# Kernel optimization log

Hardware: AMD Instinct MI355X
Metric: run time of the kernel (lower is better)

Reference implementation:

```python
import jax, jax.numpy as jnp
import numpy as np

N = 10000
F_IN = 512
HID = 256
C = 16
N_POST_ITER = 4


def setup_inputs() -> dict:
    key = jax.random.key(0)
    ks = jax.random.split(key, 10)
    raw_adj = jax.random.uniform(ks[0], (N, N), dtype=jnp.float32) * 0.01
    A = jax.random.uniform(ks[1], (N, N), dtype=jnp.float32)
    normed_adj = A / jnp.sum(A, axis=1, keepdims=True)  # row-sum-one normalized
    features = jax.random.normal(ks[2], (N, F_IN), dtype=jnp.float32)
    labels = jax.random.randint(ks[3], (N,), 0, C)
    y_onehot = jax.nn.one_hot(labels, C, dtype=jnp.float32)
    train_mask = jax.random.randint(ks[4], (N,), 0, 2).astype(jnp.bool_)
    # GCN belief estimator params (glorot-ish scaling)
    W1 = jax.random.normal(ks[5], (F_IN, HID), dtype=jnp.float32) / np.sqrt(F_IN)
    b1 = jnp.zeros((HID,), dtype=jnp.float32)
    W2 = jax.random.normal(ks[6], (HID, C), dtype=jnp.float32) / np.sqrt(HID)
    b2 = jnp.zeros((C,), dtype=jnp.float32)
    # class-compatibility matrix H (initialized, zero-centered as in init_H)
    H = jax.random.normal(ks[7], (C, C), dtype=jnp.float32) * 0.1
    return {"raw_adj": raw_adj, "normed_adj": normed_adj, "features": features,
            "y_onehot": y_onehot, "train_mask": train_mask,
            "W1": W1, "b1": b1, "W2": W2, "b2": b2, "H": H}


def reference(raw_adj, normed_adj, features, y_onehot, train_mask, W1, b1, W2, b2, H):
    num_class = y_onehot.shape[1]
    # 2-layer GCN belief estimator: adj @ (x @ W) + b
    h = jax.nn.relu(normed_adj @ (features @ W1) + b1)          # [N, HID]
    logits = normed_adj @ (h @ W2) + b2                          # [N, C]
    # post_process: iterative compatibility-guided belief propagation
    prior_belief = jax.nn.softmax(logits, axis=1)
    E_hat = prior_belief - 1.0 / num_class
    B_hat = E_hat
    for _ in range(N_POST_ITER):
        B_hat = E_hat + raw_adj @ (B_hat @ H)
    post_belief = B_hat + 1.0 / num_class
    return post_belief
```

## Files before the change

### kernel.cpp

```cpp
#include <hip/hip_runtime.h>

#define NN 10000
#define KP 10048
static constexpr float INV_C = 1.0f / 16.0f;

typedef __attribute__((ext_vector_type(8))) short bf16x8;
typedef __attribute__((ext_vector_type(4))) float f32x4;
typedef unsigned short u16;
typedef unsigned int u32;

__device__ __forceinline__ u16 f2b(float f) {
    union { float f; u32 u; } v; v.f = f;
    u32 r = v.u + 0x7FFFu + ((v.u >> 16) & 1u);
    return (u16)(r >> 16);
}
__device__ __forceinline__ float b2f(u16 b) {
    union { u32 u; float f; } v; v.u = ((u32)b) << 16;
    return v.f;
}

#define AS1(p) ((__attribute__((address_space(1))) void*)(p))
#define AS3(p) ((__attribute__((address_space(3))) void*)(p))

__global__ __launch_bounds__(256)
void cvt_pad(const float* __restrict__ src, u16* __restrict__ dst)
{
    int c8 = blockIdx.x * 256 + threadIdx.x;
    if (c8 >= KP / 8) return;
    int row = blockIdx.y;
    bf16x8 o;
    if (c8 < NN / 8) {
        const float4* s4 = (const float4*)(src + (size_t)row * NN + c8 * 8);
        float4 a = s4[0], b = s4[1];
        o[0]=f2b(a.x); o[1]=f2b(a.y); o[2]=f2b(a.z); o[3]=f2b(a.w);
        o[4]=f2b(b.x); o[5]=f2b(b.y); o[6]=f2b(b.z); o[7]=f2b(b.w);
    } else {
        o = bf16x8{0,0,0,0,0,0,0,0};
    }
    *(bf16x8*)(dst + (size_t)row * KP + c8 * 8) = o;
}

__global__ __launch_bounds__(256)
void cvt_feat(const float* __restrict__ src, u16* __restrict__ dst)
{
    int c = blockIdx.x * 256 + threadIdx.x;
    size_t base = (size_t)c * 8;
    const float4* s4 = (const float4*)(src + base);
    float4 a = s4[0], b = s4[1];
    bf16x8 o;
    o[0]=f2b(a.x); o[1]=f2b(a.y); o[2]=f2b(a.z); o[3]=f2b(a.w);
    o[4]=f2b(b.x); o[5]=f2b(b.y); o[6]=f2b(b.z); o[7]=f2b(b.w);
    *(bf16x8*)(dst + base) = o;
}

__global__ __launch_bounds__(256)
void w12t(const float* __restrict__ W1, const float* __restrict__ W2,
          float* __restrict__ W1T, u16* __restrict__ W2T)
{
    int bid = blockIdx.x, t = threadIdx.x;
    if (bid < 512) {
        int idx = bid * 256 + t;
        int n = idx >> 9, k = idx & 511;
        W1T[idx] = W1[(size_t)k * 256 + n];
    } else {
        int idx = (bid - 512) * 256 + t;
        if (idx < 4096) {
            int n_ = idx >> 8, k_ = idx & 255;
            W2T[idx] = f2b(W2[(size_t)k_ * 16 + n_]);
        }
    }
}

template<int BIAS, int RELU>
__global__ __launch_bounds__(256)
void gemm_a32_bt16(const float* __restrict__ A, int lda, int M, int Ka,
                   const u16* __restrict__ BT, int ldb, int N, int npad,
                   const float* __restrict__ bias,
                   u16* __restrict__ C, int ldc, int K)
{
    __shared__ u16 Asm[64 * 64];
    __shared__ u16 Bsm[256 * 64];
    const int t = threadIdx.x;
    const int lane = t & 63;
    const int w = t >> 6;
    const int row0 = blockIdx.x * 64;
    const int n0 = blockIdx.y * 256;

    const f32x4 fz = {0.f, 0.f, 0.f, 0.f};
    f32x4 acc[4][4];
#pragma unroll
    for (int i = 0; i < 4; ++i)
#pragma unroll
        for (int j = 0; j < 4; ++j) acc[i][j] = fz;

    const int ar = t >> 2, akq = t & 3;
    int agr = row0 + ar; if (agr > M - 1) agr = M - 1;
    const float* asrc = A + (size_t)agr * lda + akq * 16;
    const int aslot0 = (akq * 2) ^ (ar & 7);
    const int aslot1 = (akq * 2 + 1) ^ (ar & 7);

    const int l8 = lane >> 3, sl = lane & 7;

    for (int k0 = 0; k0 < K; k0 += 64) {
#pragma unroll
        for (int i = 0; i < 8; ++i) {
            int lr = i * 32 + w * 8 + l8;
            int gn = n0 + lr; if (gn > N - 1) gn = N - 1;
            int ss = sl ^ (lr & 7);
            const u16* src = BT + (size_t)gn * ldb + k0 + ss * 8;
            __builtin_amdgcn_global_load_lds(AS1(src), AS3(&Bsm[(i * 32 + w * 8) * 64]),
                                             16, 0, 0);
        }
        bool aval = (k0 + akq * 16) < Ka;
        float4 x0, x1, x2, x3;
        if (aval) {
            x0 = *(const float4*)(asrc + k0);
            x1 = *(const float4*)(asrc + k0 + 4);
            x2 = *(const float4*)(asrc + k0 + 8);
            x3 = *(const float4*)(asrc + k0 + 12);
        } else {
            x0 = x1 = x2 = x3 = make_float4(0.f, 0.f, 0.f, 0.f);
        }
        bf16x8 p0, p1;
        p0[0]=f2b(x0.x); p0[1]=f2b(x0.y); p0[2]=f2b(x0.z); p0[3]=f2b(x0.w);
        p0[4]=f2b(x1.x); p0[5]=f2b(x1.y); p0[6]=f2b(x1.z); p0[7]=f2b(x1.w);
        p1[0]=f2b(x2.x); p1[1]=f2b(x2.y); p1[2]=f2b(x2.z); p1[3]=f2b(x2.w);
        p1[4]=f2b(x3.x); p1[5]=f2b(x3.y); p1[6]=f2b(x3.z); p1[7]=f2b(x3.w);
        *(bf16x8*)&Asm[ar * 64 + aslot0 * 8] = p0;
        *(bf16x8*)&Asm[ar * 64 + aslot1 * 8] = p1;
        __syncthreads();
#pragma unroll
        for (int kk = 0; kk < 2; ++kk) {
            bf16x8 afr[4], bfr[4];
#pragma unroll
            for (int mi = 0; mi < 4; ++mi) {
                int r = mi * 16 + (lane & 15);
                int s2 = (kk * 4 + (lane >> 4)) ^ (r & 7);
                afr[mi] = *(const bf16x8*)&Asm[r * 64 + s2 * 8];
            }
#pragma unroll
            for (int ni = 0; ni < 4; ++ni) {
                int nr = w * 64 + ni * 16 + (lane & 15);
                int s2 = (kk * 4 + (lane >> 4)) ^ (nr & 7);
                bfr[ni] = *(const bf16x8*)&Bsm[nr * 64 + s2 * 8];
            }
#pragma unroll
            for (int mi = 0; mi < 4; ++mi)
#pragma unroll
                for (int ni = 0; ni < 4; ++ni)
                    acc[mi][ni] = __builtin_amdgcn_mfma_f32_16x16x32_bf16(
                        afr[mi], bfr[ni], acc[mi][ni], 0, 0, 0);
        }
        __syncthreads();
    }
#pragma unroll
    for (int mi = 0; mi < 4; ++mi) {
        int grb = row0 + mi * 16 + (lane >> 4) * 4;
#pragma unroll
        for (int ni = 0; ni < 4; ++ni) {
            int gc = n0 + w * 64 + ni * 16 + (lane & 15);
            if (gc < npad) {
                float bv = (BIAS && gc < N) ? bias[gc] : 0.f;
#pragma unroll
                for (int rg = 0; rg < 4; ++rg) {
                    int gr = grb + rg;
                    if (gr < M) {
                        float v = acc[mi][ni][rg] + bv;
                        if (RELU) v = fmaxf(v, 0.f);
                        C[(size_t)gr * ldc + gc] = f2b(gc < N ? v : 0.f);
                    }
                }
            }
        }
    }
}

template<int AFP32>
__global__ __launch_bounds__(256)
void adj16(const void* __restrict__ Av, long lda,
           const u16* __restrict__ BT,
           float* __restrict__ P, int nch, int nchf, int Kv)
{
    const int t = threadIdx.x, lane = t & 63, w = t >> 6;
    const int s = blockIdx.y;
    int row = blockIdx.x * 64 + w * 16 + (lane & 15);
    if (row > NN - 1) row = NN - 1;
    const int kq = (lane >> 4) * 8;
    const u16* brow = BT + (size_t)(lane & 15) * KP + kq;
    const float* a32 = (const float*)Av + (size_t)row * lda + kq;
    const u16*  a16 = (const u16*) Av + (size_t)row * lda + kq;

    int c0 = (nch * s) >> 3, c1 = (nch * (s + 1)) >> 3;
    int c1f = c1 < nchf ? c1 : nchf;
    f32x4 acc = {0.f, 0.f, 0.f, 0.f};
    int kc = c0;
    for (; kc + 4 <= c1f; kc += 4) {
        bf16x8 a[4], b[4];
#pragma unroll
        for (int u = 0; u < 4; ++u) {
            if (AFP32) {
                float4 x = *(const float4*)(a32 + (size_t)(kc + u) * 32);
                float4 y = *(const float4*)(a32 + (size_t)(kc + u) * 32 + 4);
                bf16x8 r;
                r[0]=f2b(x.x); r[1]=f2b(x.y); r[2]=f2b(x.z); r[3]=f2b(x.w);
                r[4]=f2b(y.x); r[5]=f2b(y.y); r[6]=f2b(y.z); r[7]=f2b(y.w);
                a[u] = r;
            } else {
                a[u] = *(const bf16x8*)(a16 + (size_t)(kc + u) * 32);
            }
            b[u] = *(const bf16x8*)(brow + (size_t)(kc + u) * 32);
        }
#pragma unroll
        for (int u = 0; u < 4; ++u)
            acc = __builtin_amdgcn_mfma_f32_16x16x32_bf16(a[u], b[u], acc, 0, 0, 0);
    }
    for (; kc < c1; ++kc) {
        bf16x8 a = bf16x8{0,0,0,0,0,0,0,0};
        if (kc < nchf || (kc * 32 + kq) < Kv) {
            if (AFP32) {
                float4 x = *(const float4*)(a32 + (size_t)kc * 32);
                float4 y = *(const float4*)(a32 + (size_t)kc * 32 + 4);
                a[0]=f2b(x.x); a[1]=f2b(x.y); a[2]=f2b(x.z); a[3]=f2b(x.w);
                a[4]=f2b(y.x); a[5]=f2b(y.y); a[6]=f2b(y.z); a[7]=f2b(y.w);
            } else {
                a = *(const bf16x8*)(a16 + (size_t)kc * 32);
            }
        }
        bf16x8 b = *(const bf16x8*)(brow + (size_t)kc * 32);
        acc = __builtin_amdgcn_mfma_f32_16x16x32_bf16(a, b, acc, 0, 0, 0);
    }
    int ob = blockIdx.x * 64 + w * 16 + (lane >> 4) * 4;
#pragma unroll
    for (int rg = 0; rg < 4; ++rg) {
        int orow = ob + rg;
        if (orow < NN)
            P[(size_t)s * (NN * 16) + (size_t)orow * 16 + (lane & 15)] = acc[rg];
    }
}

__global__ __launch_bounds__(256)
void hw2_mfma(const u16* __restrict__ h, const u16* __restrict__ W2T,
              u16* __restrict__ outT)
{
    const int t = threadIdx.x, lane = t & 63, w = t >> 6;
    int row = blockIdx.x * 64 + w * 16 + (lane & 15);
    int rowc = row < NN ? row : NN - 1;
    const int kq = (lane >> 4) * 8;
    const u16* arow = h + (size_t)rowc * 256 + kq;
    const u16* brow = W2T + (size_t)(lane & 15) * 256 + kq;
    f32x4 acc = {0.f, 0.f, 0.f, 0.f};
#pragma unroll
    for (int kc = 0; kc < 8; ++kc) {
        bf16x8 a = *(const bf16x8*)(arow + kc * 32);
        bf16x8 b = *(const bf16x8*)(brow + kc * 32);
        acc = __builtin_amdgcn_mfma_f32_16x16x32_bf16(a, b, acc, 0, 0, 0);
    }
    int ob = blockIdx.x * 64 + w * 16 + (lane >> 4) * 4;
    int col = lane & 15;
#pragma unroll
    for (int rg = 0; rg < 4; ++rg) {
        int r = ob + rg;
        outT[(size_t)col * KP + r] = f2b(r < NN ? acc[rg] : 0.f);
    }
}

__global__ __launch_bounds__(256)
void softmax_e(const float* __restrict__ P, const float* __restrict__ b2,
               float* __restrict__ E, float* __restrict__ Bout)
{
    int i = blockIdx.x * 256 + threadIdx.x;
    if (i >= NN) return;
    float l[16];
#pragma unroll
    for (int k = 0; k < 16; ++k) l[k] = b2[k];
#pragma unroll
    for (int s = 0; s < 8; ++s) {
        const float4* p4 = (const float4*)(P + (size_t)s * (NN * 16) + (size_t)i * 16);
        float4 a = p4[0], b = p4[1], c = p4[2], d = p4[3];
        l[0]+=a.x;  l[1]+=a.y;  l[2]+=a.z;  l[3]+=a.w;
        l[4]+=b.x;  l[5]+=b.y;  l[6]+=b.z;  l[7]+=b.w;
        l[8]+=c.x;  l[9]+=c.y;  l[10]+=c.z; l[11]+=c.w;
        l[12]+=d.x; l[13]+=d.y; l[14]+=d.z; l[15]+=d.w;
    }
    float mx = l[0];
#pragma unroll
    for (int k = 1; k < 16; ++k) mx = fmaxf(mx, l[k]);
    float ssum = 0.f;
#pragma unroll
    for (int k = 0; k < 16; ++k) { l[k] = __expf(l[k] - mx); ssum += l[k]; }
    float inv = 1.f / ssum;
#pragma unroll
    for (int k = 0; k < 16; ++k) {
        float e = l[k] * inv - INV_C;
        E[(size_t)i * 16 + k] = e;
        Bout[(size_t)i * 16 + k] = e;
    }
}

__global__ __launch_bounds__(256)
void bmm_h(const float* __restrict__ Bin, const float* __restrict__ H,
           u16* __restrict__ outT)
{
    __shared__ float Hs[256];
    int t = threadIdx.x;
    Hs[t] = H[t];
    __syncthreads();
    int r = blockIdx.x * 256 + t;
    if (r >= KP) return;
    float acc[16];
#pragma unroll
    for (int k = 0; k < 16; ++k) acc[k] = 0.f;
    if (r < NN) {
        const float4* b4 = (const float4*)(Bin + (size_t)r * 16);
        float4 xv[4] = {b4[0], b4[1], b4[2], b4[3]};
#pragma unroll
        for (int m = 0; m < 16; ++m) {
            float x = ((const float*)xv)[m];
            const float4* h4 = (const float4*)&Hs[m * 16];
#pragma unroll
            for (int k4 = 0; k4 < 4; ++k4) {
                float4 hh = h4[k4];
                acc[k4*4+0] += x * hh.x; acc[k4*4+1] += x * hh.y;
                acc[k4*4+2] += x * hh.z; acc[k4*4+3] += x * hh.w;
            }
        }
    }
#pragma unroll
    for (int k = 0; k < 16; ++k)
        outT[(size_t)k * KP + r] = f2b(acc[k]);
}

__global__ __launch_bounds__(256)
void combine_k(const float* __restrict__ E, const float* __restrict__ P,
               float* __restrict__ out, float addc)
{
    int i4 = blockIdx.x * 256 + threadIdx.x;
    if (i4 >= NN * 4) return;
    float4 v = ((const float4*)E)[i4];
#pragma unroll
    for (int s = 0; s < 8; ++s) {
        float4 p = ((const float4*)(P + (size_t)s * (NN * 16)))[i4];
        v.x += p.x; v.y += p.y; v.z += p.z; v.w += p.w;
    }
    v.x += addc; v.y += addc; v.z += addc; v.w += addc;
    ((float4*)out)[i4] = v;
}

extern "C" void kernel_launch(void* const* d_in, const int* in_sizes, int n_in,
                              void* d_out, int out_size, void* d_ws, size_t ws_size,
                              hipStream_t stream)
{
    const float* raw_adj    = (const float*)d_in[0];
    const float* normed_adj = (const float*)d_in[1];
    const float* features   = (const float*)d_in[2];
    const float* W1 = (const float*)d_in[5];
    const float* b1 = (const float*)d_in[6];
    const float* W2 = (const float*)d_in[7];
    const float* b2 = (const float*)d_in[8];
    const float* H  = (const float*)d_in[9];
    float* out = (float*)d_out;

    char* ws = (char*)d_ws;
    float* P      = (float*)(ws + 0);
    float* E      = (float*)(ws + 5120000);
    float* Bbuf   = (float*)(ws + 5760000);
    u16*   featbf = (u16*)  (ws + 0);
    float* W1T    = (float*)(ws + 10240000);
    u16*   W2T    = (u16*)  (ws + 10764288);
    u16*   XWT    = (u16*)  (ws + 10772480);
    u16*   hbf    = (u16*)  (ws + 15917056);
    u16*   hw2T   = (u16*)  (ws + 21037056);
    u16*   bhT    = (u16*)  (ws + 21358592);
    u16*   ArBf   = (u16*)  (ws + 21680128);
    const bool rawbf = ws_size >= (size_t)222640128;

    cvt_feat<<<2500, 256, 0, stream>>>(features, featbf);
    w12t<<<528, 256, 0, stream>>>(W1, W2, W1T, W2T);
    if (rawbf)
        cvt_pad<<<dim3(5, NN), 256, 0, stream>>>(raw_adj, ArBf);

    gemm_a32_bt16<0, 0><<<dim3(4, 40), 256, 0, stream>>>(
        W1T, 512, 256, 512, featbf, 512, NN, KP, nullptr, XWT, KP, 512);

    gemm_a32_bt16<1, 1><<<dim3(157, 1), 256, 0, stream>>>(
        normed_adj, NN, NN, NN, XWT, KP, 256, 256, b1, hbf, 256, KP);

    hw2_mfma<<<157, 256, 0, stream>>>(hbf, W2T, hw2T);

    adj16<1><<<dim3(157, 8), 256, 0, stream>>>(
        (const void*)normed_adj, NN, hw2T, P, 313, 312, NN);

    softmax_e<<<40, 256, 0, stream>>>(P, b2, E, Bbuf);

    for (int it = 0; it < 4; ++it) {
        bmm_h<<<40, 256, 0, stream>>>(Bbuf, H, bhT);
        if (rawbf)
            adj16<0><<<dim3(157, 8), 256, 0, stream>>>(
                (const void*)ArBf, KP, bhT, P, 314, 314, KP);
        else
            adj16<1><<<dim3(157, 8), 256, 0, stream>>>(
                (const void*)raw_adj, NN, bhT, P, 313, 312, NN);
        const bool last = (it == 3);
        combine_k<<<157, 256, 0, stream>>>(E, P, last ? out : Bbuf,
                                           last ? INV_C : 0.f);
    }
}
```

Baseline: 719.8 us.

## Split-K first adjacency GEMM, fuse bf16 adjacency conversion into GEMMs, merge small kernels

The first normed_adj GEMM (157 blocks, full K) becomes a split-K kernel over 8 slices with a separate reduce/bias/relu kernel, raising parallelism. Instead of a standalone cvt_pad pass over raw_adj, the first propagation iteration writes the bf16 copy as it reads, and when workspace allows the first big GEMM also writes a bf16 copy of normed_adj for the second adjacency product. Softmax is fused with the first B@H, and combine is fused with the next B@H, removing launches and an intermediate buffer. The cost is extra partial-sum traffic for split-K and extra writes inside the GEMMs.

```diff
diff --git a/kernel.cpp b/kernel.cpp
--- a/kernel.cpp
+++ b/kernel.cpp
@@ -14,31 +14,9 @@
     u32 r = v.u + 0x7FFFu + ((v.u >> 16) & 1u);
     return (u16)(r >> 16);
 }
-__device__ __forceinline__ float b2f(u16 b) {
-    union { u32 u; float f; } v; v.u = ((u32)b) << 16;
-    return v.f;
-}
 
 #define AS1(p) ((__attribute__((address_space(1))) void*)(p))
 #define AS3(p) ((__attribute__((address_space(3))) void*)(p))
-
-__global__ __launch_bounds__(256)
-void cvt_pad(const float* __restrict__ src, u16* __restrict__ dst)
-{
-    int c8 = blockIdx.x * 256 + threadIdx.x;
-    if (c8 >= KP / 8) return;
-    int row = blockIdx.y;
-    bf16x8 o;
-    if (c8 < NN / 8) {
-        const float4* s4 = (const float4*)(src + (size_t)row * NN + c8 * 8);
-        float4 a = s4[0], b = s4[1];
-        o[0]=f2b(a.x); o[1]=f2b(a.y); o[2]=f2b(a.z); o[3]=f2b(a.w);
-        o[4]=f2b(b.x); o[5]=f2b(b.y); o[6]=f2b(b.z); o[7]=f2b(b.w);
-    } else {
-        o = bf16x8{0,0,0,0,0,0,0,0};
-    }
-    *(bf16x8*)(dst + (size_t)row * KP + c8 * 8) = o;
-}
 
 __global__ __launch_bounds__(256)
 void cvt_feat(const float* __restrict__ src, u16* __restrict__ dst)
@@ -98,7 +76,6 @@
     const float* asrc = A + (size_t)agr * lda + akq * 16;
     const int aslot0 = (akq * 2) ^ (ar & 7);
     const int aslot1 = (akq * 2 + 1) ^ (ar & 7);
-
     const int l8 = lane >> 3, sl = lane & 7;
 
     for (int k0 = 0; k0 < K; k0 += 64) {
@@ -175,20 +152,150 @@
     }
 }
 
-template<int AFP32>
+template<int CVT>
+__global__ __launch_bounds__(256)
+void gemm_na(const float* __restrict__ A, const u16* __restrict__ BT,
+             float* __restrict__ Pws, u16* __restrict__ Acvt)
+{
+    __shared__ u16 Asm[64 * 64];
+    __shared__ u16 Bsm[256 * 64];
+    const int t = threadIdx.x;
+    const int lane = t & 63;
+    const int w = t >> 6;
+    const int row0 = blockIdx.x * 64;
+    const int s = blockIdx.y;
+    const int c0 = (157 * s) >> 3, c1 = (157 * (s + 1)) >> 3;
+
+    const f32x4 fz = {0.f, 0.f, 0.f, 0.f};
+    f32x4 acc[4][4];
+#pragma unroll
+    for (int i = 0; i < 4; ++i)
+#pragma unroll
+        for (int j = 0; j < 4; ++j) acc[i][j] = fz;
+
+    const int ar = t >> 2, akq = t & 3;
+    const int grow = row0 + ar;
+    const int agr = grow < NN ? grow : NN - 1;
+    const float* asrc = A + (size_t)agr * NN + akq * 16;
+    const int aslot0 = (akq * 2) ^ (ar & 7);
+    const int aslot1 = (akq * 2 + 1) ^ (ar & 7);
+    const int l8 = lane >> 3, sl = lane & 7;
+
+    for (int ck = c0; ck < c1; ++ck) {
+        const int k0 = ck * 64;
+#pragma unroll
+        for (int i = 0; i < 8; ++i) {
+            int lr = i * 32 + w * 8 + l8;
+            int ss = sl ^ (lr & 7);
+            const u16* src = BT + (size_t)lr * KP + k0 + ss * 8;
+            __builtin_amdgcn_global_load_lds(AS1(src), AS3(&Bsm[(i * 32 + w * 8) * 64]),
+                                             16, 0, 0);
+        }
+        const int kq0 = k0 + akq * 16;
+        bool aval = kq0 < NN;
+        float4 x0, x1, x2, x3;
+        if (aval) {
+            x0 = *(const float4*)(asrc + k0);
+            x1 = *(const float4*)(asrc + k0 + 4);
+            x2 = *(const float4*)(asrc + k0 + 8);
+            x3 = *(const float4*)(asrc + k0 + 12);
+        } else {
+            x0 = x1 = x2 = x3 = make_float4(0.f, 0.f, 0.f, 0.f);
+        }
+        bf16x8 p0, p1;
+        p0[0]=f2b(x0.x); p0[1]=f2b(x0.y); p0[2]=f2b(x0.z); p0[3]=f2b(x0.w);
+        p0[4]=f2b(x1.x); p0[5]=f2b(x1.y); p0[6]=f2b(x1.z); p0[7]=f2b(x1.w);
+        p1[0]=f2b(x2.x); p1[1]=f2b(x2.y); p1[2]=f2b(x2.z); p1[3]=f2b(x2.w);
+        p1[4]=f2b(x3.x); p1[5]=f2b(x3.y); p1[6]=f2b(x3.z); p1[7]=f2b(x3.w);
+        *(bf16x8*)&Asm[ar * 64 + aslot0 * 8] = p0;
+        *(bf16x8*)&Asm[ar * 64 + aslot1 * 8] = p1;
+        if (CVT && grow < NN) {
+            *(bf16x8*)(Acvt + (size_t)grow * KP + kq0) = p0;
+            *(bf16x8*)(Acvt + (size_t)grow * KP + kq0 + 8) = p1;
+        }
+        __syncthreads();
+#pragma unroll
+        for (int kk = 0; kk < 2; ++kk) {
+            bf16x8 afr[4], bfr[4];
+#pragma unroll
+            for (int mi = 0; mi < 4; ++mi) {
+                int r = mi * 16 + (lane & 15);
+                int s2 = (kk * 4 + (lane >> 4)) ^ (r & 7);
+                afr[mi] = *(const bf16x8*)&Asm[r * 64 + s2 * 8];
+            }
+#pragma unroll
+            for (int ni = 0; ni < 4; ++ni) {
+                int nr = w * 64 + ni * 16 + (lane & 15);
+                int s2 = (kk * 4 + (lane >> 4)) ^ (nr & 7);
+                bfr[ni] = *(const bf16x8*)&Bsm[nr * 64 + s2 * 8];
+            }
+#pragma unroll
+            for (int mi = 0; mi < 4; ++mi)
+#pragma unroll
+                for (int ni = 0; ni < 4; ++ni)
+                    acc[mi][ni] = __builtin_amdgcn_mfma_f32_16x16x32_bf16(
+                        afr[mi], bfr[ni], acc[mi][ni], 0, 0, 0);
+        }
+        __syncthreads();
+    }
+    float* outp = Pws + (size_t)s * NN * 256;
+#pragma unroll
+    for (int mi = 0; mi < 4; ++mi) {
+        int grb = row0 + mi * 16 + (lane >> 4) * 4;
+#pragma unroll
+        for (int ni = 0; ni < 4; ++ni) {
+            int gc = w * 64 + ni * 16 + (lane & 15);
+#pragma unroll
+            for (int rg = 0; rg < 4; ++rg) {
+                int gr = grb + rg;
+                if (gr < NN)
+                    outp[(size_t)gr * 256 + gc] = acc[mi][ni][rg];
+            }
+        }
+    }
+}
+
+__global__ __launch_bounds__(256)
+void reduce_h(const float* __restrict__ Pws, const float* __restrict__ b1,
+              u16* __restrict__ hbf)
+{
+    int i8 = blockIdx.x * 256 + threadIdx.x;
+    if (i8 >= NN * 256 / 8) return;
+    size_t base = (size_t)i8 * 8;
+    int col = (int)(base & 255);
+    float v[8];
+#pragma unroll
+    for (int j = 0; j < 8; ++j) v[j] = b1[col + j];
+#pragma unroll
+    for (int s = 0; s < 8; ++s) {
+        const float4* p = (const float4*)(Pws + (size_t)s * NN * 256 + base);
+        float4 a = p[0], b = p[1];
+        v[0]+=a.x; v[1]+=a.y; v[2]+=a.z; v[3]+=a.w;
+        v[4]+=b.x; v[5]+=b.y; v[6]+=b.z; v[7]+=b.w;
+    }
+    bf16x8 o;
+#pragma unroll
+    for (int j = 0; j < 8; ++j) o[j] = f2b(fmaxf(v[j], 0.f));
+    *(bf16x8*)(hbf + base) = o;
+}
+
+template<int AFP32, int CVT>
 __global__ __launch_bounds__(256)
 void adj16(const void* __restrict__ Av, long lda,
            const u16* __restrict__ BT,
-           float* __restrict__ P, int nch, int nchf, int Kv)
+           float* __restrict__ Pout, int nch, int nchf,
+           u16* __restrict__ Acvt)
 {
     const int t = threadIdx.x, lane = t & 63, w = t >> 6;
     const int s = blockIdx.y;
-    int row = blockIdx.x * 64 + w * 16 + (lane & 15);
-    if (row > NN - 1) row = NN - 1;
+    const int rowu = blockIdx.x * 64 + w * 16 + (lane & 15);
+    const int row = rowu < NN ? rowu : NN - 1;
     const int kq = (lane >> 4) * 8;
     const u16* brow = BT + (size_t)(lane & 15) * KP + kq;
     const float* a32 = (const float*)Av + (size_t)row * lda + kq;
     const u16*  a16 = (const u16*) Av + (size_t)row * lda + kq;
+    u16* cvtp = CVT ? (Acvt + (size_t)rowu * KP + kq) : (u16*)0;
+    const bool wok = CVT && (rowu < NN);
 
     int c0 = (nch * s) >> 3, c1 = (nch * (s + 1)) >> 3;
     int c1f = c1 < nchf ? c1 : nchf;
@@ -210,22 +317,29 @@
             }
             b[u] = *(const bf16x8*)(brow + (size_t)(kc + u) * 32);
         }
+        if (CVT && wok) {
+#pragma unroll
+            for (int u = 0; u < 4; ++u)
+                *(bf16x8*)(cvtp + (size_t)(kc + u) * 32) = a[u];
+        }
 #pragma unroll
         for (int u = 0; u < 4; ++u)
             acc = __builtin_amdgcn_mfma_f32_16x16x32_bf16(a[u], b[u], acc, 0, 0, 0);
     }
     for (; kc < c1; ++kc) {
         bf16x8 a = bf16x8{0,0,0,0,0,0,0,0};
-        if (kc < nchf || (kc * 32 + kq) < Kv) {
-            if (AFP32) {
+        if (AFP32) {
+            if (kc * 32 + kq < NN) {
                 float4 x = *(const float4*)(a32 + (size_t)kc * 32);
                 float4 y = *(const float4*)(a32 + (size_t)kc * 32 + 4);
                 a[0]=f2b(x.x); a[1]=f2b(x.y); a[2]=f2b(x.z); a[3]=f2b(x.w);
                 a[4]=f2b(y.x); a[5]=f2b(y.y); a[6]=f2b(y.z); a[7]=f2b(y.w);
-            } else {
-                a = *(const bf16x8*)(a16 + (size_t)kc * 32);
-            }
-        }
+            }
+        } else {
+            a = *(const bf16x8*)(a16 + (size_t)kc * 32);
+        }
+        if (CVT && wok)
+            *(bf16x8*)(cvtp + (size_t)kc * 32) = a;
         bf16x8 b = *(const bf16x8*)(brow + (size_t)kc * 32);
         acc = __builtin_amdgcn_mfma_f32_16x16x32_bf16(a, b, acc, 0, 0, 0);
     }
@@ -234,7 +348,7 @@
     for (int rg = 0; rg < 4; ++rg) {
         int orow = ob + rg;
         if (orow < NN)
-            P[(size_t)s * (NN * 16) + (size_t)orow * 16 + (lane & 15)] = acc[rg];
+            Pout[(size_t)s * (NN * 16) + (size_t)orow * 16 + (lane & 15)] = acc[rg];
     }
 }
 
@@ -265,57 +379,114 @@
 }
 
 __global__ __launch_bounds__(256)
-void softmax_e(const float* __restrict__ P, const float* __restrict__ b2,
-               float* __restrict__ E, float* __restrict__ Bout)
-{
-    int i = blockIdx.x * 256 + threadIdx.x;
-    if (i >= NN) return;
-    float l[16];
-#pragma unroll
-    for (int k = 0; k < 16; ++k) l[k] = b2[k];
-#pragma unroll
-    for (int s = 0; s < 8; ++s) {
-        const float4* p4 = (const float4*)(P + (size_t)s * (NN * 16) + (size_t)i * 16);
-        float4 a = p4[0], b = p4[1], c = p4[2], d = p4[3];
-        l[0]+=a.x;  l[1]+=a.y;  l[2]+=a.z;  l[3]+=a.w;
-        l[4]+=b.x;  l[5]+=b.y;  l[6]+=b.z;  l[7]+=b.w;
-        l[8]+=c.x;  l[9]+=c.y;  l[10]+=c.z; l[11]+=c.w;
-        l[12]+=d.x; l[13]+=d.y; l[14]+=d.z; l[15]+=d.w;
-    }
-    float mx = l[0];
-#pragma unroll
-    for (int k = 1; k < 16; ++k) mx = fmaxf(mx, l[k]);
-    float ssum = 0.f;
-#pragma unroll
-    for (int k = 0; k < 16; ++k) { l[k] = __expf(l[k] - mx); ssum += l[k]; }
-    float inv = 1.f / ssum;
-#pragma unroll
-    for (int k = 0; k < 16; ++k) {
-        float e = l[k] * inv - INV_C;
-        E[(size_t)i * 16 + k] = e;
-        Bout[(size_t)i * 16 + k] = e;
-    }
-}
-
-__global__ __launch_bounds__(256)
-void bmm_h(const float* __restrict__ Bin, const float* __restrict__ H,
-           u16* __restrict__ outT)
+void softmax_e_h(const float* __restrict__ P, const float* __restrict__ b2,
+                 const float* __restrict__ H, float* __restrict__ E,
+                 u16* __restrict__ bhT)
 {
     __shared__ float Hs[256];
-    int t = threadIdx.x;
+    const int t = threadIdx.x;
     Hs[t] = H[t];
     __syncthreads();
     int r = blockIdx.x * 256 + t;
     if (r >= KP) return;
+    float l[16];
+    if (r < NN) {
+#pragma unroll
+        for (int k = 0; k < 16; ++k) l[k] = b2[k];
+#pragma unroll
+        for (int s = 0; s < 8; ++s) {
+            const float4* p4 = (const float4*)(P + (size_t)s * (NN * 16) + (size_t)r * 16);
+            float4 a = p4[0], b = p4[1], c = p4[2], d = p4[3];
+            l[0]+=a.x;  l[1]+=a.y;  l[2]+=a.z;  l[3]+=a.w;
+            l[4]+=b.x;  l[5]+=b.y;  l[6]+=b.z;  l[7]+=b.w;
+            l[8]+=c.x;  l[9]+=c.y;  l[10]+=c.z; l[11]+=c.w;
+            l[12]+=d.x; l[13]+=d.y; l[14]+=d.z; l[15]+=d.w;
+        }
+        float mx = l[0];
+#pragma unroll
+        for (int k = 1; k < 16; ++k) mx = fmaxf(mx, l[k]);
+        float ssum = 0.f;
+#pragma unroll
+        for (int k = 0; k < 16; ++k) { l[k] = __expf(l[k] - mx); ssum += l[k]; }
+        float inv = 1.f / ssum;
+#pragma unroll
+        for (int k = 0; k < 16; ++k) {
+            l[k] = l[k] * inv - INV_C;
+            E[(size_t)r * 16 + k] = l[k];
+        }
+    } else {
+#pragma unroll
+        for (int k = 0; k < 16; ++k) l[k] = 0.f;
+    }
     float acc[16];
 #pragma unroll
     for (int k = 0; k < 16; ++k) acc[k] = 0.f;
+#pragma unroll
+    for (int m = 0; m < 16; ++m) {
+        float x = l[m];
+        const float4* h4 = (const float4*)&Hs[m * 16];
+#pragma unroll
+        for (int k4 = 0; k4 < 4; ++k4) {
+            float4 hh = h4[k4];
+            acc[k4*4+0] += x * hh.x; acc[k4*4+1] += x * hh.y;
+            acc[k4*4+2] += x * hh.z; acc[k4*4+3] += x * hh.w;
+        }
+    }
+#pragma unroll
+    for (int k = 0; k < 16; ++k)
+        bhT[(size_t)k * KP + r] = f2b(acc[k]);
+}
+
+template<int LAST>
+__global__ __launch_bounds__(256)
+void combine_bmm(const float* __restrict__ E, const float* __restrict__ P,
+                 const float* __restrict__ H, u16* __restrict__ bhT,
+                 float* __restrict__ out)
+{
+    __shared__ float Hs[256];
+    const int t = threadIdx.x;
+    Hs[t] = H[t];
+    __syncthreads();
+    int r = blockIdx.x * 256 + t;
+    if (r >= KP) return;
+    float Bv[16];
     if (r < NN) {
-        const float4* b4 = (const float4*)(Bin + (size_t)r * 16);
-        float4 xv[4] = {b4[0], b4[1], b4[2], b4[3]};
+        const float4* e4 = (const float4*)(E + (size_t)r * 16);
+        float4 a = e4[0], b = e4[1], c = e4[2], d = e4[3];
+        Bv[0]=a.x;  Bv[1]=a.y;  Bv[2]=a.z;  Bv[3]=a.w;
+        Bv[4]=b.x;  Bv[5]=b.y;  Bv[6]=b.z;  Bv[7]=b.w;
+        Bv[8]=c.x;  Bv[9]=c.y;  Bv[10]=c.z; Bv[11]=c.w;
+        Bv[12]=d.x; Bv[13]=d.y; Bv[14]=d.z; Bv[15]=d.w;
+#pragma unroll
+        for (int s = 0; s < 8; ++s) {
+            const float4* p4 = (const float4*)(P + (size_t)s * (NN * 16) + (size_t)r * 16);
+            float4 pa = p4[0], pb = p4[1], pc = p4[2], pd = p4[3];
+            Bv[0]+=pa.x;  Bv[1]+=pa.y;  Bv[2]+=pa.z;  Bv[3]+=pa.w;
+            Bv[4]+=pb.x;  Bv[5]+=pb.y;  Bv[6]+=pb.z;  Bv[7]+=pb.w;
+            Bv[8]+=pc.x;  Bv[9]+=pc.y;  Bv[10]+=pc.z; Bv[11]+=pc.w;
+            Bv[12]+=pd.x; Bv[13]+=pd.y; Bv[14]+=pd.z; Bv[15]+=pd.w;
+        }
+    } else {
+#pragma unroll
+        for (int k = 0; k < 16; ++k) Bv[k] = 0.f;
+    }
+    if (LAST) {
+        if (r < NN) {
+            float4 o[4];
+#pragma unroll
+            for (int q = 0; q < 4; ++q) {
+                o[q].x = Bv[q*4+0] + INV_C; o[q].y = Bv[q*4+1] + INV_C;
+                o[q].z = Bv[q*4+2] + INV_C; o[q].w = Bv[q*4+3] + INV_C;
+                ((float4*)(out + (size_t)r * 16))[q] = o[q];
+            }
+        }
+    } else {
+        float acc[16];
+#pragma unroll
+        for (int k = 0; k < 16; ++k) acc[k] = 0.f;
 #pragma unroll
         for (int m = 0; m < 16; ++m) {
-            float x = ((const float*)xv)[m];
+            float x = Bv[m];
             const float4* h4 = (const float4*)&Hs[m * 16];
 #pragma unroll
             for (int k4 = 0; k4 < 4; ++k4) {
@@ -324,26 +495,10 @@
                 acc[k4*4+2] += x * hh.z; acc[k4*4+3] += x * hh.w;
             }
         }
-    }
-#pragma unroll
-    for (int k = 0; k < 16; ++k)
-        outT[(size_t)k * KP + r] = f2b(acc[k]);
-}
-
-__global__ __launch_bounds__(256)
-void combine_k(const float* __restrict__ E, const float* __restrict__ P,
-               float* __restrict__ out, float addc)
-{
-    int i4 = blockIdx.x * 256 + threadIdx.x;
-    if (i4 >= NN * 4) return;
-    float4 v = ((const float4*)E)[i4];
-#pragma unroll
-    for (int s = 0; s < 8; ++s) {
-        float4 p = ((const float4*)(P + (size_t)s * (NN * 16)))[i4];
-        v.x += p.x; v.y += p.y; v.z += p.z; v.w += p.w;
-    }
-    v.x += addc; v.y += addc; v.z += addc; v.w += addc;
-    ((float4*)out)[i4] = v;
+#pragma unroll
+        for (int k = 0; k < 16; ++k)
+            bhT[(size_t)k * KP + r] = f2b(acc[k]);
+    }
 }
 
 extern "C" void kernel_launch(void* const* d_in, const int* in_sizes, int n_in,
@@ -361,47 +516,65 @@
     float* out = (float*)d_out;
 
     char* ws = (char*)d_ws;
+    u16*   featbf = (u16*)  (ws + 0);
     float* P      = (float*)(ws + 0);
     float* E      = (float*)(ws + 5120000);
-    float* Bbuf   = (float*)(ws + 5760000);
-    u16*   featbf = (u16*)  (ws + 0);
     float* W1T    = (float*)(ws + 10240000);
     u16*   W2T    = (u16*)  (ws + 10764288);
     u16*   XWT    = (u16*)  (ws + 10772480);
     u16*   hbf    = (u16*)  (ws + 15917056);
     u16*   hw2T   = (u16*)  (ws + 21037056);
     u16*   bhT    = (u16*)  (ws + 21358592);
-    u16*   ArBf   = (u16*)  (ws + 21680128);
-    const bool rawbf = ws_size >= (size_t)222640128;
+    const bool full  = ws_size >= (size_t)304560128;
+    const bool mid   = ws_size >= (size_t)222640128;
+    const bool low   = ws_size >= (size_t)103600128;
+    u16*   An_bf = (u16*)  (ws + 21680128);
+    float* Pws   = (float*)(ws + (full ? 222640128 : 21680128));
+    u16*   ArBf  = (u16*)  (ws + 21680128);
 
     cvt_feat<<<2500, 256, 0, stream>>>(features, featbf);
     w12t<<<528, 256, 0, stream>>>(W1, W2, W1T, W2T);
-    if (rawbf)
-        cvt_pad<<<dim3(5, NN), 256, 0, stream>>>(raw_adj, ArBf);
 
     gemm_a32_bt16<0, 0><<<dim3(4, 40), 256, 0, stream>>>(
         W1T, 512, 256, 512, featbf, 512, NN, KP, nullptr, XWT, KP, 512);
 
-    gemm_a32_bt16<1, 1><<<dim3(157, 1), 256, 0, stream>>>(
-        normed_adj, NN, NN, NN, XWT, KP, 256, 256, b1, hbf, 256, KP);
+    if (low) {
+        if (full)
+            gemm_na<1><<<dim3(157, 8), 256, 0, stream>>>(normed_adj, XWT, Pws, An_bf);
+        else
+            gemm_na<0><<<dim3(157, 8), 256, 0, stream>>>(normed_adj, XWT, Pws, nullptr);
+        reduce_h<<<1250, 256, 0, stream>>>(Pws, b1, hbf);
+    } else {
+        gemm_a32_bt16<1, 1><<<dim3(157, 1), 256, 0, stream>>>(
+            normed_adj, NN, NN, NN, XWT, KP, 256, 256, b1, hbf, 256, KP);
+    }
 
     hw2_mfma<<<157, 256, 0, stream>>>(hbf, W2T, hw2T);
 
-    adj16<1><<<dim3(157, 8), 256, 0, stream>>>(
-        (const void*)normed_adj, NN, hw2T, P, 313, 312, NN);
-
-    softmax_e<<<40, 256, 0, stream>>>(P, b2, E, Bbuf);
+    if (full)
+        adj16<0, 0><<<dim3(157, 8), 256, 0, stream>>>(
+            (const void*)An_bf, KP, hw2T, P, 314, 314, nullptr);
+    else
+        adj16<1, 0><<<dim3(157, 8), 256, 0, stream>>>(
+            (const void*)normed_adj, NN, hw2T, P, 313, 312, nullptr);
+
+    softmax_e_h<<<40, 256, 0, stream>>>(P, b2, H, E, bhT);
 
     for (int it = 0; it < 4; ++it) {
-        bmm_h<<<40, 256, 0, stream>>>(Bbuf, H, bhT);
-        if (rawbf)
-            adj16<0><<<dim3(157, 8), 256, 0, stream>>>(
-                (const void*)ArBf, KP, bhT, P, 314, 314, KP);
+        if (mid) {
+            if (it == 0)
+                adj16<1, 1><<<dim3(157, 8), 256, 0, stream>>>(
+                    (const void*)raw_adj, NN, bhT, P, 314, 312, ArBf);
+            else
+                adj16<0, 0><<<dim3(157, 8), 256, 0, stream>>>(
+                    (const void*)ArBf, KP, bhT, P, 314, 314, nullptr);
+        } else {
+            adj16<1, 0><<<dim3(157, 8), 256, 0, stream>>>(
+                (const void*)raw_adj, NN, bhT, P, 313, 312, nullptr);
+        }
+        if (it == 3)
+            combine_bmm<1><<<40, 256, 0, stream>>>(E, P, H, nullptr, out);
         else
-            adj16<1><<<dim3(157, 8), 256, 0, stream>>>(
-                (const void*)raw_adj, NN, bhT, P, 313, 312, NN);
-        const bool last = (it == 3);
-        combine_k<<<157, 256, 0, stream>>>(E, P, last ? out : Bbuf,
-                                           last ? INV_C : 0.f);
-    }
-}
+            combine_bmm<0><<<40, 256, 0, stream>>>(E, P, H, bhT, nullptr);
+    }
+}
```

Result: faster. 609.1 us (-15.4%).
